# Kernel tuning notes

Measured on AMD Instinct MI355X. Metric: run time of the kernel, lower is better.

Reference implementation:

```python
import jax, jax.numpy as jnp
import numpy as np

# static config (matches init_kwargs)
T_K = 3      # Time_kernel
K = 3        # spatial_kernel_side_length
C = 64       # dim_hidden
H = 4        # num_head
D = 16       # dim_head
NL = 2       # num_layers
F = 3        # dim_feature
N, S1, S2 = 32, 32, 32
P = K // 2
L1 = T_K // 2
M = T_K * K * K
EPS = 1e-5


def _neighbor_mask():
    # spatial_neighbor_mask with an all-ones city mask: offset (k1,k2) is a valid
    # neighbor of cell (s1,s2) iff it lands inside the grid.
    m = np.zeros((S1, S2, K, K), dtype=bool)
    s1 = np.arange(S1); s2 = np.arange(S2)
    for k1 in range(K):
        v1 = (s1 + k1 - P >= 0) & (s1 + k1 - P < S1)
        for k2 in range(K):
            v2 = (s2 + k2 - P >= 0) & (s2 + k2 - P < S2)
            m[:, :, k1, k2] = v1[:, None] & v2[None, :]
    mf = m.reshape(S1, S2, K * K)
    # tiled across Time_kernel, flattened in (t, k1, k2) order like the torch code
    return np.tile(mf[:, :, None, :], (1, 1, T_K, 1)).reshape(S1, S2, M)

_MASK = jnp.asarray(_neighbor_mask())


def _forward(x, W_in, b_in, W_out, b_out, Wq, bq, Wk, bk, Wv, bv):
    # BatchNorm2d (training-mode batch stats, affine = identity init)
    mean = x.mean(axis=(0, 1, 2))
    var = ((x - mean) ** 2).mean(axis=(0, 1, 2))
    h = (x - mean) * jax.lax.rsqrt(var + EPS)
    h = h @ W_in + b_in  # [N,S1,S2,C]

    for l in range(NL):
        res = h  # res_block_thickness = 1 -> residual every layer
        q = (h @ Wq[l] + bq[l]).reshape(N, S1, S2, H, D)
        # spatial unfold (nn.Unfold, padding=K//2, stride=1)
        hp = jnp.pad(h, ((0, 0), (P, P), (P, P), (0, 0)))
        u = jnp.stack([jnp.stack([hp[:, k1:k1 + S1, k2:k2 + S2, :]
                                  for k2 in range(K)]) for k1 in range(K)])  # [K,K,N,S1,S2,C]
        # time unfold (zero-padded shifts along N)
        up = jnp.pad(u, ((0, 0), (0, 0), (L1, L1), (0, 0), (0, 0), (0, 0)))
        ut = jnp.stack([up[:, :, t:t + N] for t in range(T_K)])  # [T,K,K,N,S1,S2,C]
        # per-offset single-Linear MLPs (kernel_neurons=[C,C]), batched over T,K,K
        ks = jnp.einsum('tijnabc,tijcd->nabtijd', ut, Wk[l]) + bk[l]
        vs = jnp.einsum('tijnabc,tijcd->nabtijd', ut, Wv[l]) + bv[l]
        kM = ks.reshape(N, S1, S2, M, H, D)
        vM = vs.reshape(N, S1, S2, M, H, D)
        # unscaled dot-product attention over valid neighbors (masked == dropped)
        sc = jnp.einsum('nabmhd,nabhd->nabhm', kM, q)
        sc = jnp.where(_MASK[None, :, :, None, :], sc, -1e30)
        w = jax.nn.softmax(sc, axis=-1)
        h = jnp.einsum('nabhm,nabmhd->nabhd', w, vM).reshape(N, S1, S2, C)
        h = h + res

    return h @ W_out + b_out  # [N,S1,S2,F]


def setup_inputs() -> dict:
    key = jax.random.key(0)
    k = jax.random.split(key, 11)
    s = 0.05
    return {
        'x': jax.random.normal(k[0], (N, S1, S2, F), jnp.float32),
        'W_in': jax.random.normal(k[1], (F, C), jnp.float32) * s,
        'b_in': jax.random.normal(k[2], (C,), jnp.float32) * s,
        'W_out': jax.random.normal(k[3], (C, F), jnp.float32) * s,
        'b_out': jax.random.normal(k[4], (F,), jnp.float32) * s,
        'Wq': jax.random.normal(k[5], (NL, C, C), jnp.float32) * s,
        'bq': jax.random.normal(k[6], (NL, C), jnp.float32) * s,
        'Wk': jax.random.normal(k[7], (NL, T_K, K, K, C, C), jnp.float32) * s,
        'bk': jax.random.normal(k[8], (NL, T_K, K, K, C), jnp.float32) * s,
        'Wv': jax.random.normal(k[9], (NL, T_K, K, K, C, C), jnp.float32) * s,
        'bv': jax.random.normal(k[10], (NL, T_K, K, K, C), jnp.float32) * s,
    }


def reference(x, W_in, b_in, W_out, b_out, Wq, bq, Wk, bk, Wv, bv):
    return _forward(x, W_in, b_in, W_out, b_out, Wq, bq, Wk, bk, Wv, bv)
```

## Files before the change

### kernel.cpp

```cpp
#include <hip/hip_runtime.h>
#include <hip/hip_bf16.h>


typedef short short8_t __attribute__((ext_vector_type(8)));
typedef float floatx16 __attribute__((ext_vector_type(16)));

__device__ __forceinline__ short f2bs(float f) {
    __hip_bfloat16 h = __float2bfloat16(f);
    return *reinterpret_cast<short*>(&h);
}
__device__ __forceinline__ float bs2f(short s) {
    union { unsigned u; float f; } v;
    v.u = ((unsigned)(unsigned short)s) << 16;
    return v.f;
}
__device__ __forceinline__ int hn_idx(int rowid, int chunk) {
    return rowid * 64 + ((chunk ^ (rowid & 7)) << 3);
}
__device__ __forceinline__ float half_sum(float p) {
    float a = p, b = p;
    asm("v_permlane32_swap_b32 %0, %1" : "+v"(a), "+v"(b));
    return a + b;
}

__global__ void prep_kernel(const float* __restrict__ Wq, const float* __restrict__ Wk,
                            const float* __restrict__ Wv, short* __restrict__ dst,
                            const float* __restrict__ x, float* __restrict__ sums) {
    if (blockIdx.x < 220) {
        int t = blockIdx.x * 256 + threadIdx.x;
        if (t >= 110 * 512) return;
        int mat  = t >> 9;
        int rem  = t & 511;
        int hp   = rem >> 8;
        int kk   = (rem >> 6) & 3;
        int lane = rem & 63;
        int krow = kk * 16 + ((lane >> 5) << 3);
        int col  = hp * 32 + (lane & 31);
        const float* W;
        if (mat < 2)       W = Wq + mat * 4096;
        else if (mat < 56) W = Wk + (mat - 2) * 4096;
        else               W = Wv + (mat - 56) * 4096;
        short8_t v;
        #pragma unroll
        for (int j = 0; j < 8; ++j) v[j] = f2bs(W[(krow + j) * 64 + col]);
        *(short8_t*)&dst[(size_t)mat * 4096 + ((hp * 4 + kk) * 64 + lane) * 8] = v;
    } else {
        int bid = blockIdx.x - 220;
        int t = bid * 256 + threadIdx.x;
        const float4* x4 = (const float4*)x;
        float4 v0 = x4[t * 3 + 0], v1 = x4[t * 3 + 1], v2 = x4[t * 3 + 2];
        float vv[6];
        vv[0] = v0.x + v0.w + v1.z + v2.y;
        vv[1] = v0.y + v1.x + v1.w + v2.z;
        vv[2] = v0.z + v1.y + v2.x + v2.w;
        vv[3] = v0.x*v0.x + v0.w*v0.w + v1.z*v1.z + v2.y*v2.y;
        vv[4] = v0.y*v0.y + v1.x*v1.x + v1.w*v1.w + v2.z*v2.z;
        vv[5] = v0.z*v0.z + v1.y*v1.y + v2.x*v2.x + v2.w*v2.w;
        #pragma unroll
        for (int i = 0; i < 6; ++i) {
            #pragma unroll
            for (int off = 1; off < 64; off <<= 1) vv[i] += __shfl_xor(vv[i], off);
        }
        __shared__ float part[4][6];
        if ((threadIdx.x & 63) == 0) {
            #pragma unroll
            for (int i = 0; i < 6; ++i) part[threadIdx.x >> 6][i] = vv[i];
        }
        __syncthreads();
        if (threadIdx.x < 6)
            sums[bid * 8 + threadIdx.x] = part[0][threadIdx.x] + part[1][threadIdx.x] +
                                          part[2][threadIdx.x] + part[3][threadIdx.x];
    }
}

template <bool FIRST>
__global__ __launch_bounds__(512, 4)
void layer_fused(const float* __restrict__ x, const float* __restrict__ sums,
                 const float* __restrict__ W_in, const float* __restrict__ b_in,
                 const short* __restrict__ hbf_in, short* __restrict__ hbf_out,
                 const float* __restrict__ Wout, const float* __restrict__ bout,
                 float* __restrict__ out,
                 const short* __restrict__ wqB, const float* __restrict__ bq,
                 const short* __restrict__ wkB, const float* __restrict__ bk,
                 const short* __restrict__ wvB, const float* __restrict__ bv) {
    __shared__ short HnS[216 * 64];
    __shared__ float BiasS[3456];
    __shared__ float Waux[256];
    __shared__ float bn6[6];

    const int tid = threadIdx.x;
    const int bb0 = blockIdx.x * 2, a = blockIdx.y, nb = blockIdx.z;

    if (FIRST) {
        if (tid < 3) {
            float s = 0.f, qq = 0.f;
            #pragma unroll
            for (int p = 0; p < 32; ++p) { s += sums[p * 8 + tid]; qq += sums[p * 8 + 3 + tid]; }
            float mean = s * (1.f / 32768.f);
            float var  = qq * (1.f / 32768.f) - mean * mean;
            bn6[tid]     = mean;
            bn6[3 + tid] = rsqrtf(var + 1e-5f);
        }
        if (tid < 192)      Waux[tid] = W_in[tid];
        else if (tid < 256) Waux[tid] = b_in[tid - 192];
    } else {
        if (tid < 192)      Waux[tid] = Wout[tid];
        else if (tid < 195) Waux[tid] = bout[tid - 192];
    }
    __syncthreads();

    float mean0 = 0, mean1 = 0, mean2 = 0, rs0 = 0, rs1 = 0, rs2 = 0;
    if (FIRST) {
        mean0 = bn6[0]; mean1 = bn6[1]; mean2 = bn6[2];
        rs0 = bn6[3]; rs1 = bn6[4]; rs2 = bn6[5];
    }

    for (int id = tid; id < 3456; id += 512) {
        const int half = (id >= 1728) ? 1 : 0;
        const int j = id - half * 1728;
        const float* src = half ? &bv[j] : &bk[j];
        BiasS[((j >> 6) << 7) + (half << 6) + (j & 63)] = *src;
    }

    for (int id = tid; id < 1728; id += 512) {
        int rowid = id >> 3, cc = id & 7;
        int r = rowid % 18;
        int rw = rowid / 18;
        int spa = rw >> 2, jcol = rw & 3;
        int aa = a + spa - 1, bb = bb0 + jcol - 1;
        int n  = nb * 16 + r - 1;
        short8_t v = {0, 0, 0, 0, 0, 0, 0, 0};
        if ((unsigned)n < 32u && (unsigned)aa < 32u && (unsigned)bb < 32u) {
            int cell = (n * 32 + aa) * 32 + bb;
            if (FIRST) {
                float xn0 = (x[cell*3+0] - mean0) * rs0;
                float xn1 = (x[cell*3+1] - mean1) * rs1;
                float xn2 = (x[cell*3+2] - mean2) * rs2;
                #pragma unroll
                for (int j = 0; j < 8; ++j) {
                    int c = cc * 8 + j;
                    float h = Waux[192+c] + xn0*Waux[c] + xn1*Waux[64+c] + xn2*Waux[128+c];
                    v[j] = f2bs(h);
                }
            } else {
                v = *(const short8_t*)&hbf_in[cell * 64 + cc * 8];
            }
        }
        *(short8_t*)&HnS[hn_idx(rowid, cc)] = v;
    }
    __syncthreads();

    const int lane = tid & 63;
    const int wv8  = tid >> 6;
    const int hp   = wv8 & 1;
    const int g4   = wv8 >> 1;
    const int col  = lane & 31;
    const int e    = col & 15;
    const int ci   = col >> 4;
    const int h5   = lane >> 5;

    unsigned amask = 0;
    #pragma unroll
    for (int d = 0; d < 3; ++d) if ((unsigned)(a + d - 1) < 32u) amask |= 1u << d;
    const bool vbL = (unsigned)(bb0 - 1) < 32u;
    const bool vbR = (unsigned)(bb0 + 2) < 32u;
    const unsigned vmask = (ci == 0) ? ((vbL ? 1u : 0u) | 2u | 4u)
                                     : (1u | 2u | (vbR ? 4u : 0u));

    const int elane = e + ci * 18;

    floatx16 qv;
    {
        const float* bqp = &bq[hp * 32 + 4 * h5];
        const float4 qa = *(const float4*)&bqp[0];
        const float4 qb = *(const float4*)&bqp[8];
        const float4 qc = *(const float4*)&bqp[16];
        const float4 qd = *(const float4*)&bqp[24];
        qv = floatx16{qa.x,qa.y,qa.z,qa.w, qb.x,qb.y,qb.z,qb.w,
                      qc.x,qc.y,qc.z,qc.w, qd.x,qd.y,qd.z,qd.w};
        const int hrow = (5 + ci) * 18 + e + 1;
        const int hb = hrow * 64, xr = hrow & 7;
        const short8_t b0 = *(const short8_t*)&HnS[hb + (((0 + h5) ^ xr) << 3)];
        const short8_t b1 = *(const short8_t*)&HnS[hb + (((2 + h5) ^ xr) << 3)];
        const short8_t b2 = *(const short8_t*)&HnS[hb + (((4 + h5) ^ xr) << 3)];
        const short8_t b3 = *(const short8_t*)&HnS[hb + (((6 + h5) ^ xr) << 3)];
        const short8_t* wqp = (const short8_t*)&wqB[(hp * 256 + lane) * 8];
        qv = __builtin_amdgcn_mfma_f32_32x32x16_bf16(wqp[0],   b0, qv, 0, 0, 0);
        qv = __builtin_amdgcn_mfma_f32_32x32x16_bf16(wqp[64],  b1, qv, 0, 0, 0);
        qv = __builtin_amdgcn_mfma_f32_32x32x16_bf16(wqp[128], b2, qv, 0, 0, 0);
        qv = __builtin_amdgcn_mfma_f32_32x32x16_bf16(wqp[192], b3, qv, 0, 0, 0);
    }

    floatx16 o = {0,0,0,0, 0,0,0,0, 0,0,0,0, 0,0,0,0};
    float ssA = 0.f, ssB = 0.f;

    const int mstart = g4 * 7;
    const int mend   = (g4 == 3) ? 27 : mstart + 7;

    const short* wkBase = wkB + hp * 2048 + lane * 8;
    const short* wvBase = wvB + hp * 2048 + lane * 8;

    short8_t wkX[4], wkY[4];
    #pragma unroll
    for (int j = 0; j < 4; ++j)
        wkX[j] = *(const short8_t*)&wkBase[mstart * 4096 + j * 512];

    auto body = [&](short8_t (&wkc)[4], short8_t (&wkn)[4], const int m) {
        const int mn = (m + 1 < mend) ? (m + 1) : m;
        const int t  = (m * 57) >> 9;
        const int sp = m - 9 * t;
        const int di = (sp * 11) >> 5;
        const int dj = sp - 3 * di;

        const int hrow = (di * 4 + dj) * 18 + t + elane;
        const int hb = hrow * 64, xr = hrow & 7;
        const short8_t b0 = *(const short8_t*)&HnS[hb + (((0 + h5) ^ xr) << 3)];
        const short8_t b1 = *(const short8_t*)&HnS[hb + (((2 + h5) ^ xr) << 3)];
        const short8_t b2 = *(const short8_t*)&HnS[hb + (((4 + h5) ^ xr) << 3)];
        const short8_t b3 = *(const short8_t*)&HnS[hb + (((6 + h5) ^ xr) << 3)];

        const float* bks = &BiasS[(m << 7) + (hp << 5) + (h5 << 2)];
        const float4 ka = *(const float4*)&bks[0];
        const float4 kb = *(const float4*)&bks[8];
        const float4 kc = *(const float4*)&bks[16];
        const float4 kd = *(const float4*)&bks[24];
        const float4 va0 = *(const float4*)&bks[64];
        const float4 va1 = *(const float4*)&bks[72];
        const float4 va2 = *(const float4*)&bks[80];
        const float4 va3 = *(const float4*)&bks[88];

        const short8_t wv0 = *(const short8_t*)&wvBase[m * 4096 + 0];
        const short8_t wv1 = *(const short8_t*)&wvBase[m * 4096 + 512];
        const short8_t wv2 = *(const short8_t*)&wvBase[m * 4096 + 1024];
        const short8_t wv3 = *(const short8_t*)&wvBase[m * 4096 + 1536];

        #pragma unroll
        for (int j = 0; j < 4; ++j)
            wkn[j] = *(const short8_t*)&wkBase[mn * 4096 + j * 512];

        floatx16 kacc = floatx16{ka.x,ka.y,ka.z,ka.w, kb.x,kb.y,kb.z,kb.w,
                                 kc.x,kc.y,kc.z,kc.w, kd.x,kd.y,kd.z,kd.w};
        kacc = __builtin_amdgcn_mfma_f32_32x32x16_bf16(wkc[0], b0, kacc, 0, 0, 0);
        kacc = __builtin_amdgcn_mfma_f32_32x32x16_bf16(wkc[1], b1, kacc, 0, 0, 0);
        kacc = __builtin_amdgcn_mfma_f32_32x32x16_bf16(wkc[2], b2, kacc, 0, 0, 0);
        kacc = __builtin_amdgcn_mfma_f32_32x32x16_bf16(wkc[3], b3, kacc, 0, 0, 0);

        floatx16 vacc = floatx16{va0.x,va0.y,va0.z,va0.w, va1.x,va1.y,va1.z,va1.w,
                                 va2.x,va2.y,va2.z,va2.w, va3.x,va3.y,va3.z,va3.w};
        vacc = __builtin_amdgcn_mfma_f32_32x32x16_bf16(wv0, b0, vacc, 0, 0, 0);
        vacc = __builtin_amdgcn_mfma_f32_32x32x16_bf16(wv1, b1, vacc, 0, 0, 0);
        vacc = __builtin_amdgcn_mfma_f32_32x32x16_bf16(wv2, b2, vacc, 0, 0, 0);
        vacc = __builtin_amdgcn_mfma_f32_32x32x16_bf16(wv3, b3, vacc, 0, 0, 0);

        float pA = kacc[0] * qv[0];
        #pragma unroll
        for (int r = 1; r < 8; ++r) pA += kacc[r] * qv[r];
        float pB = kacc[8] * qv[8];
        #pragma unroll
        for (int r = 9; r < 16; ++r) pB += kacc[r] * qv[r];
        pA = half_sum(pA);
        pB = half_sum(pB);
        const float mf = (float)(((amask >> di) & (vmask >> dj)) & 1u);
        const float wA = __expf(pA) * mf;
        const float wB = __expf(pB) * mf;
        ssA += wA; ssB += wB;
        #pragma unroll
        for (int r = 0; r < 8; ++r)  o[r] += wA * vacc[r];
        #pragma unroll
        for (int r = 8; r < 16; ++r) o[r] += wB * vacc[r];
    };

    for (int m = mstart; m < mend; m += 2) {
        body(wkX, wkY, m);
        if (m + 1 < mend) body(wkY, wkX, m + 1);
    }

    __syncthreads();
    float* stbuf = (float*)HnS;
    if (g4 >= 2) {
        float* d = &stbuf[(((g4 - 2) * 2 + hp) * 64 + lane) * 20];
        *(float4*)&d[0]  = make_float4(o[0],  o[1],  o[2],  o[3]);
        *(float4*)&d[4]  = make_float4(o[4],  o[5],  o[6],  o[7]);
        *(float4*)&d[8]  = make_float4(o[8],  o[9],  o[10], o[11]);
        *(float4*)&d[12] = make_float4(o[12], o[13], o[14], o[15]);
        *(float2*)&d[16] = make_float2(ssA, ssB);
    }
    __syncthreads();
    if (g4 < 2) {
        const float* d = &stbuf[((g4 * 2 + hp) * 64 + lane) * 20];
        const float4 r0 = *(const float4*)&d[0];
        const float4 r1 = *(const float4*)&d[4];
        const float4 r2 = *(const float4*)&d[8];
        const float4 r3 = *(const float4*)&d[12];
        const float2 rs = *(const float2*)&d[16];
        o[0] += r0.x; o[1] += r0.y; o[2]  += r0.z; o[3]  += r0.w;
        o[4] += r1.x; o[5] += r1.y; o[6]  += r1.z; o[7]  += r1.w;
        o[8] += r2.x; o[9] += r2.y; o[10] += r2.z; o[11] += r2.w;
        o[12] += r3.x; o[13] += r3.y; o[14] += r3.z; o[15] += r3.w;
        ssA += rs.x; ssB += rs.y;
    }
    __syncthreads();
    if (g4 == 1) {
        float* d = &stbuf[(hp * 64 + lane) * 20];
        *(float4*)&d[0]  = make_float4(o[0],  o[1],  o[2],  o[3]);
        *(float4*)&d[4]  = make_float4(o[4],  o[5],  o[6],  o[7]);
        *(float4*)&d[8]  = make_float4(o[8],  o[9],  o[10], o[11]);
        *(float4*)&d[12] = make_float4(o[12], o[13], o[14], o[15]);
        *(float2*)&d[16] = make_float2(ssA, ssB);
    }
    __syncthreads();
    if (g4 == 0) {
        const float* d = &stbuf[(hp * 64 + lane) * 20];
        const float4 r0 = *(const float4*)&d[0];
        const float4 r1 = *(const float4*)&d[4];
        const float4 r2 = *(const float4*)&d[8];
        const float4 r3 = *(const float4*)&d[12];
        const float2 rs = *(const float2*)&d[16];
        o[0] += r0.x; o[1] += r0.y; o[2]  += r0.z; o[3]  += r0.w;
        o[4] += r1.x; o[5] += r1.y; o[6]  += r1.z; o[7]  += r1.w;
        o[8] += r2.x; o[9] += r2.y; o[10] += r2.z; o[11] += r2.w;
        o[12] += r3.x; o[13] += r3.y; o[14] += r3.z; o[15] += r3.w;
        ssA += rs.x; ssB += rs.y;
        const float invA = 1.0f / ssA;
        const float invB = 1.0f / ssB;
        #pragma unroll
        for (int r = 0; r < 8; ++r)  o[r] *= invA;
        #pragma unroll
        for (int r = 8; r < 16; ++r) o[r] *= invB;
    }

    const int n = nb * 16 + e;
    if (FIRST) {
        if (g4 == 0) {
            const int cell = (n * 32 + a) * 32 + bb0 + ci;
            const float xn0 = (x[cell*3+0] - mean0) * rs0;
            const float xn1 = (x[cell*3+1] - mean1) * rs1;
            const float xn2 = (x[cell*3+2] - mean2) * rs2;
            #pragma unroll
            for (int g = 0; g < 4; ++g) {
                short4 hb4; short* hbp = (short*)&hb4;
                #pragma unroll
                for (int i = 0; i < 4; ++i) {
                    const int c = hp * 32 + g * 8 + 4 * h5 + i;
                    const float res = Waux[192+c] + xn0*Waux[c] + xn1*Waux[64+c] + xn2*Waux[128+c];
                    hbp[i] = f2bs(o[g * 4 + i] + res);
                }
                *(short4*)&hbf_out[cell * 64 + hp * 32 + g * 8 + 4 * h5] = hb4;
            }
        }
    } else {
        __syncthreads();
        float* hf = (float*)HnS;
        if (g4 == 0) {
            const int cell = (n * 32 + a) * 32 + bb0 + ci;
            #pragma unroll
            for (int g = 0; g < 4; ++g) {
                const short4 hb4 = *(const short4*)&hbf_in[cell * 64 + hp * 32 + g * 8 + 4 * h5];
                float4 tv = make_float4(o[g*4+0] + bs2f(hb4.x), o[g*4+1] + bs2f(hb4.y),
                                        o[g*4+2] + bs2f(hb4.z), o[g*4+3] + bs2f(hb4.w));
                *(float4*)&hf[col * 68 + hp * 32 + g * 8 + 4 * h5] = tv;
            }
        }
        __syncthreads();
        if (tid < 384) {
            const int oid = tid >> 2, part = tid & 3;
            const int rowglob = oid / 3, f = oid - rowglob * 3;
            const int cstart = part << 4;
            float acc = 0.f;
            #pragma unroll
            for (int cc = 0; cc < 16; ++cc)
                acc += hf[rowglob * 68 + cstart + cc] * Waux[(cstart + cc) * 3 + f];
            acc += __shfl_xor(acc, 1);
            acc += __shfl_xor(acc, 2);
            if (part == 0) {
                const int cio = rowglob >> 4, row = rowglob & 15;
                out[(((nb * 16 + row) * 32 + a) * 32 + bb0 + cio) * 3 + f] =
                    acc + Waux[192 + f];
            }
        }
    }
}

extern "C" void kernel_launch(void* const* d_in, const int* in_sizes, int n_in,
                              void* d_out, int out_size, void* d_ws, size_t ws_size,
                              hipStream_t stream) {
    const float* x     = (const float*)d_in[0];
    const float* W_in  = (const float*)d_in[1];
    const float* b_in  = (const float*)d_in[2];
    const float* W_out = (const float*)d_in[3];
    const float* b_out = (const float*)d_in[4];
    const float* Wq    = (const float*)d_in[5];
    const float* bq    = (const float*)d_in[6];
    const float* Wk    = (const float*)d_in[7];
    const float* bk    = (const float*)d_in[8];
    const float* Wv    = (const float*)d_in[9];
    const float* bv    = (const float*)d_in[10];

    float* ws    = (float*)d_ws;
    float* sums  = ws;
    short* h1bf  = (short*)(ws + 256);
    short* wB    = h1bf + 2097152;
    float* out   = (float*)d_out;

    prep_kernel<<<252, 256, 0, stream>>>(Wq, Wk, Wv, wB, x, sums);

    const short* wq0 = wB;                const short* wq1 = wB + 4096;
    const short* wk0 = wB + 2 * 4096;     const short* wk1 = wB + (2 + 27) * 4096;
    const short* wv0 = wB + 56 * 4096;    const short* wv1 = wB + (56 + 27) * 4096;

    dim3 grid(16, 32, 2);
    layer_fused<true><<<grid, 512, 0, stream>>>(
        x, sums, W_in, b_in, nullptr, h1bf, nullptr, nullptr, nullptr,
        wq0, bq, wk0, bk, wv0, bv);
    layer_fused<false><<<grid, 512, 0, stream>>>(
        nullptr, nullptr, nullptr, nullptr, h1bf, nullptr, W_out, b_out, out,
        wq1, bq + 64, wk1, bk + 1728, wv1, bv + 1728);
}
```

Baseline: 143.4 us.

## Prefetch both K and V weights one step ahead; stage prep weights through LDS

The main loop now double-buffers the V weight fragments as well as the K fragments, loading the next offset's Wk and Wv while the current MFMAs run, so global-load latency is hidden behind compute. Launch bounds drop from 4 to 3 waves per SIMD to make room for the extra registers, which lowers occupancy. The prep kernel now uses one block per matrix, staging the matrix in shared memory with coalesced float4 loads before the strided bf16 repack, and the grid shrinks to match.

```diff
diff --git a/kernel.cpp b/kernel.cpp
--- a/kernel.cpp
+++ b/kernel.cpp
@@ -26,26 +26,33 @@
 __global__ void prep_kernel(const float* __restrict__ Wq, const float* __restrict__ Wk,
                             const float* __restrict__ Wv, short* __restrict__ dst,
                             const float* __restrict__ x, float* __restrict__ sums) {
-    if (blockIdx.x < 220) {
-        int t = blockIdx.x * 256 + threadIdx.x;
-        if (t >= 110 * 512) return;
-        int mat  = t >> 9;
-        int rem  = t & 511;
-        int hp   = rem >> 8;
-        int kk   = (rem >> 6) & 3;
-        int lane = rem & 63;
-        int krow = kk * 16 + ((lane >> 5) << 3);
-        int col  = hp * 32 + (lane & 31);
+    if (blockIdx.x < 110) {
+        __shared__ float Wf[4096];
+        const int mat = blockIdx.x;
         const float* W;
         if (mat < 2)       W = Wq + mat * 4096;
         else if (mat < 56) W = Wk + (mat - 2) * 4096;
         else               W = Wv + (mat - 56) * 4096;
-        short8_t v;
+        const float4* W4 = (const float4*)W;
         #pragma unroll
-        for (int j = 0; j < 8; ++j) v[j] = f2bs(W[(krow + j) * 64 + col]);
-        *(short8_t*)&dst[(size_t)mat * 4096 + ((hp * 4 + kk) * 64 + lane) * 8] = v;
+        for (int i = 0; i < 4; ++i) {
+            const int idx = threadIdx.x + i * 256;
+            *(float4*)&Wf[idx * 4] = W4[idx];
+        }
+        __syncthreads();
+        #pragma unroll
+        for (int u = 0; u < 2; ++u) {
+            const int t2 = u * 256 + threadIdx.x;
+            const int hp = t2 >> 8, kk = (t2 >> 6) & 3, lane = t2 & 63;
+            const int krow = kk * 16 + ((lane >> 5) << 3);
+            const int col  = hp * 32 + (lane & 31);
+            short8_t v;
+            #pragma unroll
+            for (int j = 0; j < 8; ++j) v[j] = f2bs(Wf[(krow + j) * 64 + col]);
+            *(short8_t*)&dst[(size_t)mat * 4096 + t2 * 8] = v;
+        }
     } else {
-        int bid = blockIdx.x - 220;
+        int bid = blockIdx.x - 110;
         int t = bid * 256 + threadIdx.x;
         const float4* x4 = (const float4*)x;
         float4 v0 = x4[t * 3 + 0], v1 = x4[t * 3 + 1], v2 = x4[t * 3 + 2];
@@ -74,7 +81,7 @@
 }
 
 template <bool FIRST>
-__global__ __launch_bounds__(512, 4)
+__global__ __launch_bounds__(512, 3)
 void layer_fused(const float* __restrict__ x, const float* __restrict__ sums,
                  const float* __restrict__ W_in, const float* __restrict__ b_in,
                  const short* __restrict__ hbf_in, short* __restrict__ hbf_out,
@@ -200,80 +207,89 @@
     const short* wkBase = wkB + hp * 2048 + lane * 8;
     const short* wvBase = wvB + hp * 2048 + lane * 8;
 
-    short8_t wkX[4], wkY[4];
-    #pragma unroll
-    for (int j = 0; j < 4; ++j)
-        wkX[j] = *(const short8_t*)&wkBase[mstart * 4096 + j * 512];
-
-    auto body = [&](short8_t (&wkc)[4], short8_t (&wkn)[4], const int m) {
-        const int mn = (m + 1 < mend) ? (m + 1) : m;
-        const int t  = (m * 57) >> 9;
-        const int sp = m - 9 * t;
-        const int di = (sp * 11) >> 5;
-        const int dj = sp - 3 * di;
-
-        const int hrow = (di * 4 + dj) * 18 + t + elane;
-        const int hb = hrow * 64, xr = hrow & 7;
-        const short8_t b0 = *(const short8_t*)&HnS[hb + (((0 + h5) ^ xr) << 3)];
-        const short8_t b1 = *(const short8_t*)&HnS[hb + (((2 + h5) ^ xr) << 3)];
-        const short8_t b2 = *(const short8_t*)&HnS[hb + (((4 + h5) ^ xr) << 3)];
-        const short8_t b3 = *(const short8_t*)&HnS[hb + (((6 + h5) ^ xr) << 3)];
-
-        const float* bks = &BiasS[(m << 7) + (hp << 5) + (h5 << 2)];
-        const float4 ka = *(const float4*)&bks[0];
-        const float4 kb = *(const float4*)&bks[8];
-        const float4 kc = *(const float4*)&bks[16];
-        const float4 kd = *(const float4*)&bks[24];
-        const float4 va0 = *(const float4*)&bks[64];
-        const float4 va1 = *(const float4*)&bks[72];
-        const float4 va2 = *(const float4*)&bks[80];
-        const float4 va3 = *(const float4*)&bks[88];
-
-        const short8_t wv0 = *(const short8_t*)&wvBase[m * 4096 + 0];
-        const short8_t wv1 = *(const short8_t*)&wvBase[m * 4096 + 512];
-        const short8_t wv2 = *(const short8_t*)&wvBase[m * 4096 + 1024];
-        const short8_t wv3 = *(const short8_t*)&wvBase[m * 4096 + 1536];
-
-        #pragma unroll
-        for (int j = 0; j < 4; ++j)
-            wkn[j] = *(const short8_t*)&wkBase[mn * 4096 + j * 512];
-
-        floatx16 kacc = floatx16{ka.x,ka.y,ka.z,ka.w, kb.x,kb.y,kb.z,kb.w,
-                                 kc.x,kc.y,kc.z,kc.w, kd.x,kd.y,kd.z,kd.w};
-        kacc = __builtin_amdgcn_mfma_f32_32x32x16_bf16(wkc[0], b0, kacc, 0, 0, 0);
-        kacc = __builtin_amdgcn_mfma_f32_32x32x16_bf16(wkc[1], b1, kacc, 0, 0, 0);
-        kacc = __builtin_amdgcn_mfma_f32_32x32x16_bf16(wkc[2], b2, kacc, 0, 0, 0);
-        kacc = __builtin_amdgcn_mfma_f32_32x32x16_bf16(wkc[3], b3, kacc, 0, 0, 0);
-
-        floatx16 vacc = floatx16{va0.x,va0.y,va0.z,va0.w, va1.x,va1.y,va1.z,va1.w,
-                                 va2.x,va2.y,va2.z,va2.w, va3.x,va3.y,va3.z,va3.w};
-        vacc = __builtin_amdgcn_mfma_f32_32x32x16_bf16(wv0, b0, vacc, 0, 0, 0);
-        vacc = __builtin_amdgcn_mfma_f32_32x32x16_bf16(wv1, b1, vacc, 0, 0, 0);
-        vacc = __builtin_amdgcn_mfma_f32_32x32x16_bf16(wv2, b2, vacc, 0, 0, 0);
-        vacc = __builtin_amdgcn_mfma_f32_32x32x16_bf16(wv3, b3, vacc, 0, 0, 0);
-
-        float pA = kacc[0] * qv[0];
-        #pragma unroll
-        for (int r = 1; r < 8; ++r) pA += kacc[r] * qv[r];
-        float pB = kacc[8] * qv[8];
-        #pragma unroll
-        for (int r = 9; r < 16; ++r) pB += kacc[r] * qv[r];
-        pA = half_sum(pA);
-        pB = half_sum(pB);
-        const float mf = (float)(((amask >> di) & (vmask >> dj)) & 1u);
-        const float wA = __expf(pA) * mf;
-        const float wB = __expf(pB) * mf;
-        ssA += wA; ssB += wB;
-        #pragma unroll
-        for (int r = 0; r < 8; ++r)  o[r] += wA * vacc[r];
-        #pragma unroll
-        for (int r = 8; r < 16; ++r) o[r] += wB * vacc[r];
-    };
+    short8_t wkP0, wkP1, wkP2, wkP3, wvP0, wvP1, wvP2, wvP3;
+    short8_t wkQ0, wkQ1, wkQ2, wkQ3, wvQ0, wvQ1, wvQ2, wvQ3;
+    wkP0 = *(const short8_t*)&wkBase[mstart * 4096 + 0];
+    wkP1 = *(const short8_t*)&wkBase[mstart * 4096 + 512];
+    wkP2 = *(const short8_t*)&wkBase[mstart * 4096 + 1024];
+    wkP3 = *(const short8_t*)&wkBase[mstart * 4096 + 1536];
+    wvP0 = *(const short8_t*)&wvBase[mstart * 4096 + 0];
+    wvP1 = *(const short8_t*)&wvBase[mstart * 4096 + 512];
+    wvP2 = *(const short8_t*)&wvBase[mstart * 4096 + 1024];
+    wvP3 = *(const short8_t*)&wvBase[mstart * 4096 + 1536];
+
+#define KV_BODY(WKC0,WKC1,WKC2,WKC3, WVC0,WVC1,WVC2,WVC3,                          \
+                WKN0,WKN1,WKN2,WKN3, WVN0,WVN1,WVN2,WVN3, MV)                      \
+    {                                                                              \
+        const int m_  = (MV);                                                      \
+        const int mn_ = (m_ + 1 < mend) ? m_ + 1 : m_;                             \
+        const int t_  = (m_ * 57) >> 9;                                            \
+        const int sp_ = m_ - 9 * t_;                                               \
+        const int di_ = (sp_ * 11) >> 5;                                           \
+        const int dj_ = sp_ - 3 * di_;                                             \
+        const int hrow_ = (di_ * 4 + dj_) * 18 + t_ + elane;                       \
+        const int hb_ = hrow_ * 64, xr_ = hrow_ & 7;                               \
+        const short8_t b0_ = *(const short8_t*)&HnS[hb_ + (((0 + h5) ^ xr_) << 3)];\
+        const short8_t b1_ = *(const short8_t*)&HnS[hb_ + (((2 + h5) ^ xr_) << 3)];\
+        const short8_t b2_ = *(const short8_t*)&HnS[hb_ + (((4 + h5) ^ xr_) << 3)];\
+        const short8_t b3_ = *(const short8_t*)&HnS[hb_ + (((6 + h5) ^ xr_) << 3)];\
+        const float* bks_ = &BiasS[(m_ << 7) + (hp << 5) + (h5 << 2)];             \
+        const float4 ka_ = *(const float4*)&bks_[0];                               \
+        const float4 kb_ = *(const float4*)&bks_[8];                               \
+        const float4 kc_ = *(const float4*)&bks_[16];                              \
+        const float4 kd_ = *(const float4*)&bks_[24];                              \
+        const float4 va0_ = *(const float4*)&bks_[64];                             \
+        const float4 va1_ = *(const float4*)&bks_[72];                             \
+        const float4 va2_ = *(const float4*)&bks_[80];                             \
+        const float4 va3_ = *(const float4*)&bks_[88];                             \
+        WKN0 = *(const short8_t*)&wkBase[mn_ * 4096 + 0];                          \
+        WKN1 = *(const short8_t*)&wkBase[mn_ * 4096 + 512];                        \
+        WKN2 = *(const short8_t*)&wkBase[mn_ * 4096 + 1024];                       \
+        WKN3 = *(const short8_t*)&wkBase[mn_ * 4096 + 1536];                       \
+        WVN0 = *(const short8_t*)&wvBase[mn_ * 4096 + 0];                          \
+        WVN1 = *(const short8_t*)&wvBase[mn_ * 4096 + 512];                        \
+        WVN2 = *(const short8_t*)&wvBase[mn_ * 4096 + 1024];                       \
+        WVN3 = *(const short8_t*)&wvBase[mn_ * 4096 + 1536];                       \
+        floatx16 kacc_ = floatx16{ka_.x,ka_.y,ka_.z,ka_.w, kb_.x,kb_.y,kb_.z,kb_.w,\
+                                  kc_.x,kc_.y,kc_.z,kc_.w, kd_.x,kd_.y,kd_.z,kd_.w};\
+        kacc_ = __builtin_amdgcn_mfma_f32_32x32x16_bf16(WKC0, b0_, kacc_, 0, 0, 0);\
+        kacc_ = __builtin_amdgcn_mfma_f32_32x32x16_bf16(WKC1, b1_, kacc_, 0, 0, 0);\
+        kacc_ = __builtin_amdgcn_mfma_f32_32x32x16_bf16(WKC2, b2_, kacc_, 0, 0, 0);\
+        kacc_ = __builtin_amdgcn_mfma_f32_32x32x16_bf16(WKC3, b3_, kacc_, 0, 0, 0);\
+        floatx16 vacc_ = floatx16{va0_.x,va0_.y,va0_.z,va0_.w,                     \
+                                  va1_.x,va1_.y,va1_.z,va1_.w,                     \
+                                  va2_.x,va2_.y,va2_.z,va2_.w,                     \
+                                  va3_.x,va3_.y,va3_.z,va3_.w};                    \
+        vacc_ = __builtin_amdgcn_mfma_f32_32x32x16_bf16(WVC0, b0_, vacc_, 0, 0, 0);\
+        vacc_ = __builtin_amdgcn_mfma_f32_32x32x16_bf16(WVC1, b1_, vacc_, 0, 0, 0);\
+        vacc_ = __builtin_amdgcn_mfma_f32_32x32x16_bf16(WVC2, b2_, vacc_, 0, 0, 0);\
+        vacc_ = __builtin_amdgcn_mfma_f32_32x32x16_bf16(WVC3, b3_, vacc_, 0, 0, 0);\
+        float pA_ = kacc_[0] * qv[0];                                              \
+        _Pragma("unroll")                                                          \
+        for (int r = 1; r < 8; ++r) pA_ += kacc_[r] * qv[r];                       \
+        float pB_ = kacc_[8] * qv[8];                                              \
+        _Pragma("unroll")                                                          \
+        for (int r = 9; r < 16; ++r) pB_ += kacc_[r] * qv[r];                      \
+        pA_ = half_sum(pA_);                                                       \
+        pB_ = half_sum(pB_);                                                       \
+        const float mf_ = (float)(((amask >> di_) & (vmask >> dj_)) & 1u);         \
+        const float wA_ = __expf(pA_) * mf_;                                       \
+        const float wB_ = __expf(pB_) * mf_;                                       \
+        ssA += wA_; ssB += wB_;                                                    \
+        _Pragma("unroll")                                                          \
+        for (int r = 0; r < 8; ++r)  o[r] += wA_ * vacc_[r];                       \
+        _Pragma("unroll")                                                          \
+        for (int r = 8; r < 16; ++r) o[r] += wB_ * vacc_[r];                       \
+    }
 
     for (int m = mstart; m < mend; m += 2) {
-        body(wkX, wkY, m);
-        if (m + 1 < mend) body(wkY, wkX, m + 1);
-    }
+        KV_BODY(wkP0,wkP1,wkP2,wkP3, wvP0,wvP1,wvP2,wvP3,
+                wkQ0,wkQ1,wkQ2,wkQ3, wvQ0,wvQ1,wvQ2,wvQ3, m)
+        if (m + 1 < mend)
+        KV_BODY(wkQ0,wkQ1,wkQ2,wkQ3, wvQ0,wvQ1,wvQ2,wvQ3,
+                wkP0,wkP1,wkP2,wkP3, wvP0,wvP1,wvP2,wvP3, m + 1)
+    }
+#undef KV_BODY
 
     __syncthreads();
     float* stbuf = (float*)HnS;
@@ -402,7 +418,7 @@
     short* wB    = h1bf + 2097152;
     float* out   = (float*)d_out;
 
-    prep_kernel<<<252, 256, 0, stream>>>(Wq, Wk, Wv, wB, x, sums);
+    prep_kernel<<<142, 256, 0, stream>>>(Wq, Wk, Wv, wB, x, sums);
 
     const short* wq0 = wB;                const short* wq1 = wB + 4096;
     const short* wk0 = wB + 2 * 4096;     const short* wk1 = wB + (2 + 27) * 4096;
```

Result: slower. 153.3 us (+6.9%).

## Give each wave full offset loop over more cells instead of splitting offsets

Applied to the files above, without the earlier changes.

The layer kernel drops the split of the 27 neighbour offsets across four wave groups and the LDS tree reduction that merged their partial outputs. Each block now handles four columns with 256 threads, and each wave loops over all 27 offsets for its own cells, using a larger halo tile in LDS. This removes the cross-wave reduction syncs and the extra LDS traffic, and halves the grid, at the cost of a longer serial loop per wave, fewer blocks, and dropping the explicit wk register prefetch. The prep kernel now stages each weight matrix through LDS with coalesced float4 loads before repacking it to bf16.

```diff
diff --git a/kernel.cpp b/kernel.cpp
--- a/kernel.cpp
+++ b/kernel.cpp
@@ -26,26 +26,33 @@
 __global__ void prep_kernel(const float* __restrict__ Wq, const float* __restrict__ Wk,
                             const float* __restrict__ Wv, short* __restrict__ dst,
                             const float* __restrict__ x, float* __restrict__ sums) {
-    if (blockIdx.x < 220) {
-        int t = blockIdx.x * 256 + threadIdx.x;
-        if (t >= 110 * 512) return;
-        int mat  = t >> 9;
-        int rem  = t & 511;
-        int hp   = rem >> 8;
-        int kk   = (rem >> 6) & 3;
-        int lane = rem & 63;
-        int krow = kk * 16 + ((lane >> 5) << 3);
-        int col  = hp * 32 + (lane & 31);
+    if (blockIdx.x < 110) {
+        __shared__ float Wf[4096];
+        const int mat = blockIdx.x;
         const float* W;
         if (mat < 2)       W = Wq + mat * 4096;
         else if (mat < 56) W = Wk + (mat - 2) * 4096;
         else               W = Wv + (mat - 56) * 4096;
-        short8_t v;
-        #pragma unroll
-        for (int j = 0; j < 8; ++j) v[j] = f2bs(W[(krow + j) * 64 + col]);
-        *(short8_t*)&dst[(size_t)mat * 4096 + ((hp * 4 + kk) * 64 + lane) * 8] = v;
+        const float4* W4 = (const float4*)W;
+        #pragma unroll
+        for (int i = 0; i < 4; ++i) {
+            const int idx = threadIdx.x + i * 256;
+            *(float4*)&Wf[idx * 4] = W4[idx];
+        }
+        __syncthreads();
+        #pragma unroll
+        for (int u = 0; u < 2; ++u) {
+            const int t2 = u * 256 + threadIdx.x;
+            const int hp = t2 >> 8, kk = (t2 >> 6) & 3, lane = t2 & 63;
+            const int krow = kk * 16 + ((lane >> 5) << 3);
+            const int col  = hp * 32 + (lane & 31);
+            short8_t v;
+            #pragma unroll
+            for (int j = 0; j < 8; ++j) v[j] = f2bs(Wf[(krow + j) * 64 + col]);
+            *(short8_t*)&dst[(size_t)mat * 4096 + t2 * 8] = v;
+        }
     } else {
-        int bid = blockIdx.x - 220;
+        int bid = blockIdx.x - 110;
         int t = bid * 256 + threadIdx.x;
         const float4* x4 = (const float4*)x;
         float4 v0 = x4[t * 3 + 0], v1 = x4[t * 3 + 1], v2 = x4[t * 3 + 2];
@@ -74,7 +81,7 @@
 }
 
 template <bool FIRST>
-__global__ __launch_bounds__(512, 4)
+__global__ __launch_bounds__(256, 2)
 void layer_fused(const float* __restrict__ x, const float* __restrict__ sums,
                  const float* __restrict__ W_in, const float* __restrict__ b_in,
                  const short* __restrict__ hbf_in, short* __restrict__ hbf_out,
@@ -83,13 +90,13 @@
                  const short* __restrict__ wqB, const float* __restrict__ bq,
                  const short* __restrict__ wkB, const float* __restrict__ bk,
                  const short* __restrict__ wvB, const float* __restrict__ bv) {
-    __shared__ short HnS[216 * 64];
+    __shared__ short HnS[324 * 64];
     __shared__ float BiasS[3456];
     __shared__ float Waux[256];
     __shared__ float bn6[6];
 
     const int tid = threadIdx.x;
-    const int bb0 = blockIdx.x * 2, a = blockIdx.y, nb = blockIdx.z;
+    const int bb0 = blockIdx.x * 4, a = blockIdx.y, nb = blockIdx.z;
 
     if (FIRST) {
         if (tid < 3) {
@@ -101,8 +108,8 @@
             bn6[tid]     = mean;
             bn6[3 + tid] = rsqrtf(var + 1e-5f);
         }
-        if (tid < 192)      Waux[tid] = W_in[tid];
-        else if (tid < 256) Waux[tid] = b_in[tid - 192];
+        if (tid < 192) Waux[tid] = W_in[tid];
+        else           Waux[tid] = b_in[tid - 192];
     } else {
         if (tid < 192)      Waux[tid] = Wout[tid];
         else if (tid < 195) Waux[tid] = bout[tid - 192];
@@ -115,18 +122,18 @@
         rs0 = bn6[3]; rs1 = bn6[4]; rs2 = bn6[5];
     }
 
-    for (int id = tid; id < 3456; id += 512) {
+    for (int id = tid; id < 3456; id += 256) {
         const int half = (id >= 1728) ? 1 : 0;
         const int j = id - half * 1728;
         const float* src = half ? &bv[j] : &bk[j];
         BiasS[((j >> 6) << 7) + (half << 6) + (j & 63)] = *src;
     }
 
-    for (int id = tid; id < 1728; id += 512) {
+    for (int id = tid; id < 2592; id += 256) {
         int rowid = id >> 3, cc = id & 7;
         int r = rowid % 18;
         int rw = rowid / 18;
-        int spa = rw >> 2, jcol = rw & 3;
+        int spa = rw / 6, jcol = rw - spa * 6;
         int aa = a + spa - 1, bb = bb0 + jcol - 1;
         int n  = nb * 16 + r - 1;
         short8_t v = {0, 0, 0, 0, 0, 0, 0, 0};
@@ -151,23 +158,24 @@
     __syncthreads();
 
     const int lane = tid & 63;
-    const int wv8  = tid >> 6;
-    const int hp   = wv8 & 1;
-    const int g4   = wv8 >> 1;
+    const int wv4  = tid >> 6;
+    const int hp   = wv4 & 1;
+    const int cg   = wv4 >> 1;
     const int col  = lane & 31;
     const int e    = col & 15;
     const int ci   = col >> 4;
     const int h5   = lane >> 5;
+    const int cell4 = cg * 2 + ci;
+    const int bcell = bb0 + cell4;
 
     unsigned amask = 0;
     #pragma unroll
     for (int d = 0; d < 3; ++d) if ((unsigned)(a + d - 1) < 32u) amask |= 1u << d;
-    const bool vbL = (unsigned)(bb0 - 1) < 32u;
-    const bool vbR = (unsigned)(bb0 + 2) < 32u;
-    const unsigned vmask = (ci == 0) ? ((vbL ? 1u : 0u) | 2u | 4u)
-                                     : (1u | 2u | (vbR ? 4u : 0u));
-
-    const int elane = e + ci * 18;
+    unsigned vmask = 0;
+    #pragma unroll
+    for (int j = 0; j < 3; ++j) if ((unsigned)(bcell + j - 1) < 32u) vmask |= 1u << j;
+
+    const int elane = cell4 * 18 + e;
 
     floatx16 qv;
     {
@@ -178,7 +186,7 @@
         const float4 qd = *(const float4*)&bqp[24];
         qv = floatx16{qa.x,qa.y,qa.z,qa.w, qb.x,qb.y,qb.z,qb.w,
                       qc.x,qc.y,qc.z,qc.w, qd.x,qd.y,qd.z,qd.w};
-        const int hrow = (5 + ci) * 18 + e + 1;
+        const int hrow = (7 + cell4) * 18 + e + 1;
         const int hb = hrow * 64, xr = hrow & 7;
         const short8_t b0 = *(const short8_t*)&HnS[hb + (((0 + h5) ^ xr) << 3)];
         const short8_t b1 = *(const short8_t*)&HnS[hb + (((2 + h5) ^ xr) << 3)];
@@ -194,25 +202,17 @@
     floatx16 o = {0,0,0,0, 0,0,0,0, 0,0,0,0, 0,0,0,0};
     float ssA = 0.f, ssB = 0.f;
 
-    const int mstart = g4 * 7;
-    const int mend   = (g4 == 3) ? 27 : mstart + 7;
-
     const short* wkBase = wkB + hp * 2048 + lane * 8;
     const short* wvBase = wvB + hp * 2048 + lane * 8;
 
-    short8_t wkX[4], wkY[4];
-    #pragma unroll
-    for (int j = 0; j < 4; ++j)
-        wkX[j] = *(const short8_t*)&wkBase[mstart * 4096 + j * 512];
-
-    auto body = [&](short8_t (&wkc)[4], short8_t (&wkn)[4], const int m) {
-        const int mn = (m + 1 < mend) ? (m + 1) : m;
+    #pragma unroll 3
+    for (int m = 0; m < 27; ++m) {
         const int t  = (m * 57) >> 9;
         const int sp = m - 9 * t;
         const int di = (sp * 11) >> 5;
         const int dj = sp - 3 * di;
 
-        const int hrow = (di * 4 + dj) * 18 + t + elane;
+        const int hrow = di * 108 + dj * 18 + t + elane;
         const int hb = hrow * 64, xr = hrow & 7;
         const short8_t b0 = *(const short8_t*)&HnS[hb + (((0 + h5) ^ xr) << 3)];
         const short8_t b1 = *(const short8_t*)&HnS[hb + (((2 + h5) ^ xr) << 3)];
@@ -229,21 +229,21 @@
         const float4 va2 = *(const float4*)&bks[80];
         const float4 va3 = *(const float4*)&bks[88];
 
+        const short8_t wk0 = *(const short8_t*)&wkBase[m * 4096 + 0];
+        const short8_t wk1 = *(const short8_t*)&wkBase[m * 4096 + 512];
+        const short8_t wk2 = *(const short8_t*)&wkBase[m * 4096 + 1024];
+        const short8_t wk3 = *(const short8_t*)&wkBase[m * 4096 + 1536];
         const short8_t wv0 = *(const short8_t*)&wvBase[m * 4096 + 0];
         const short8_t wv1 = *(const short8_t*)&wvBase[m * 4096 + 512];
         const short8_t wv2 = *(const short8_t*)&wvBase[m * 4096 + 1024];
         const short8_t wv3 = *(const short8_t*)&wvBase[m * 4096 + 1536];
 
-        #pragma unroll
-        for (int j = 0; j < 4; ++j)
-            wkn[j] = *(const short8_t*)&wkBase[mn * 4096 + j * 512];
-
         floatx16 kacc = floatx16{ka.x,ka.y,ka.z,ka.w, kb.x,kb.y,kb.z,kb.w,
                                  kc.x,kc.y,kc.z,kc.w, kd.x,kd.y,kd.z,kd.w};
-        kacc = __builtin_amdgcn_mfma_f32_32x32x16_bf16(wkc[0], b0, kacc, 0, 0, 0);
-        kacc = __builtin_amdgcn_mfma_f32_32x32x16_bf16(wkc[1], b1, kacc, 0, 0, 0);
-        kacc = __builtin_amdgcn_mfma_f32_32x32x16_bf16(wkc[2], b2, kacc, 0, 0, 0);
-        kacc = __builtin_amdgcn_mfma_f32_32x32x16_bf16(wkc[3], b3, kacc, 0, 0, 0);
+        kacc = __builtin_amdgcn_mfma_f32_32x32x16_bf16(wk0, b0, kacc, 0, 0, 0);
+        kacc = __builtin_amdgcn_mfma_f32_32x32x16_bf16(wk1, b1, kacc, 0, 0, 0);
+        kacc = __builtin_amdgcn_mfma_f32_32x32x16_bf16(wk2, b2, kacc, 0, 0, 0);
+        kacc = __builtin_amdgcn_mfma_f32_32x32x16_bf16(wk3, b3, kacc, 0, 0, 0);
 
         floatx16 vacc = floatx16{va0.x,va0.y,va0.z,va0.w, va1.x,va1.y,va1.z,va1.w,
                                  va2.x,va2.y,va2.z,va2.w, va3.x,va3.y,va3.z,va3.w};
@@ -268,59 +268,9 @@
         for (int r = 0; r < 8; ++r)  o[r] += wA * vacc[r];
         #pragma unroll
         for (int r = 8; r < 16; ++r) o[r] += wB * vacc[r];
-    };
-
-    for (int m = mstart; m < mend; m += 2) {
-        body(wkX, wkY, m);
-        if (m + 1 < mend) body(wkY, wkX, m + 1);
-    }
-
-    __syncthreads();
-    float* stbuf = (float*)HnS;
-    if (g4 >= 2) {
-        float* d = &stbuf[(((g4 - 2) * 2 + hp) * 64 + lane) * 20];
-        *(float4*)&d[0]  = make_float4(o[0],  o[1],  o[2],  o[3]);
-        *(float4*)&d[4]  = make_float4(o[4],  o[5],  o[6],  o[7]);
-        *(float4*)&d[8]  = make_float4(o[8],  o[9],  o[10], o[11]);
-        *(float4*)&d[12] = make_float4(o[12], o[13], o[14], o[15]);
-        *(float2*)&d[16] = make_float2(ssA, ssB);
-    }
-    __syncthreads();
-    if (g4 < 2) {
-        const float* d = &stbuf[((g4 * 2 + hp) * 64 + lane) * 20];
-        const float4 r0 = *(const float4*)&d[0];
-        const float4 r1 = *(const float4*)&d[4];
-        const float4 r2 = *(const float4*)&d[8];
-        const float4 r3 = *(const float4*)&d[12];
-        const float2 rs = *(const float2*)&d[16];
-        o[0] += r0.x; o[1] += r0.y; o[2]  += r0.z; o[3]  += r0.w;
-        o[4] += r1.x; o[5] += r1.y; o[6]  += r1.z; o[7]  += r1.w;
-        o[8] += r2.x; o[9] += r2.y; o[10] += r2.z; o[11] += r2.w;
-        o[12] += r3.x; o[13] += r3.y; o[14] += r3.z; o[15] += r3.w;
-        ssA += rs.x; ssB += rs.y;
-    }
-    __syncthreads();
-    if (g4 == 1) {
-        float* d = &stbuf[(hp * 64 + lane) * 20];
-        *(float4*)&d[0]  = make_float4(o[0],  o[1],  o[2],  o[3]);
-        *(float4*)&d[4]  = make_float4(o[4],  o[5],  o[6],  o[7]);
-        *(float4*)&d[8]  = make_float4(o[8],  o[9],  o[10], o[11]);
-        *(float4*)&d[12] = make_float4(o[12], o[13], o[14], o[15]);
-        *(float2*)&d[16] = make_float2(ssA, ssB);
-    }
-    __syncthreads();
-    if (g4 == 0) {
-        const float* d = &stbuf[(hp * 64 + lane) * 20];
-        const float4 r0 = *(const float4*)&d[0];
-        const float4 r1 = *(const float4*)&d[4];
-        const float4 r2 = *(const float4*)&d[8];
-        const float4 r3 = *(const float4*)&d[12];
-        const float2 rs = *(const float2*)&d[16];
-        o[0] += r0.x; o[1] += r0.y; o[2]  += r0.z; o[3]  += r0.w;
-        o[4] += r1.x; o[5] += r1.y; o[6]  += r1.z; o[7]  += r1.w;
-        o[8] += r2.x; o[9] += r2.y; o[10] += r2.z; o[11] += r2.w;
-        o[12] += r3.x; o[13] += r3.y; o[14] += r3.z; o[15] += r3.w;
-        ssA += rs.x; ssB += rs.y;
+    }
+
+    {
         const float invA = 1.0f / ssA;
         const float invB = 1.0f / ssB;
         #pragma unroll
@@ -330,53 +280,41 @@
     }
 
     const int n = nb * 16 + e;
+    const int cell = (n * 32 + a) * 32 + bcell;
     if (FIRST) {
-        if (g4 == 0) {
-            const int cell = (n * 32 + a) * 32 + bb0 + ci;
-            const float xn0 = (x[cell*3+0] - mean0) * rs0;
-            const float xn1 = (x[cell*3+1] - mean1) * rs1;
-            const float xn2 = (x[cell*3+2] - mean2) * rs2;
-            #pragma unroll
-            for (int g = 0; g < 4; ++g) {
-                short4 hb4; short* hbp = (short*)&hb4;
-                #pragma unroll
-                for (int i = 0; i < 4; ++i) {
-                    const int c = hp * 32 + g * 8 + 4 * h5 + i;
-                    const float res = Waux[192+c] + xn0*Waux[c] + xn1*Waux[64+c] + xn2*Waux[128+c];
-                    hbp[i] = f2bs(o[g * 4 + i] + res);
-                }
-                *(short4*)&hbf_out[cell * 64 + hp * 32 + g * 8 + 4 * h5] = hb4;
+        const float xn0 = (x[cell*3+0] - mean0) * rs0;
+        const float xn1 = (x[cell*3+1] - mean1) * rs1;
+        const float xn2 = (x[cell*3+2] - mean2) * rs2;
+        #pragma unroll
+        for (int g = 0; g < 4; ++g) {
+            short4 hb4; short* hbp = (short*)&hb4;
+            #pragma unroll
+            for (int i = 0; i < 4; ++i) {
+                const int c = hp * 32 + g * 8 + 4 * h5 + i;
+                const float res = Waux[192+c] + xn0*Waux[c] + xn1*Waux[64+c] + xn2*Waux[128+c];
+                hbp[i] = f2bs(o[g * 4 + i] + res);
             }
+            *(short4*)&hbf_out[cell * 64 + hp * 32 + g * 8 + 4 * h5] = hb4;
         }
     } else {
         __syncthreads();
         float* hf = (float*)HnS;
-        if (g4 == 0) {
-            const int cell = (n * 32 + a) * 32 + bb0 + ci;
-            #pragma unroll
-            for (int g = 0; g < 4; ++g) {
-                const short4 hb4 = *(const short4*)&hbf_in[cell * 64 + hp * 32 + g * 8 + 4 * h5];
-                float4 tv = make_float4(o[g*4+0] + bs2f(hb4.x), o[g*4+1] + bs2f(hb4.y),
-                                        o[g*4+2] + bs2f(hb4.z), o[g*4+3] + bs2f(hb4.w));
-                *(float4*)&hf[col * 68 + hp * 32 + g * 8 + 4 * h5] = tv;
-            }
+        const int bcol = cell4 * 16 + e;
+        #pragma unroll
+        for (int g = 0; g < 4; ++g) {
+            const short4 hb4 = *(const short4*)&hbf_in[cell * 64 + hp * 32 + g * 8 + 4 * h5];
+            float4 tv = make_float4(o[g*4+0] + bs2f(hb4.x), o[g*4+1] + bs2f(hb4.y),
+                                    o[g*4+2] + bs2f(hb4.z), o[g*4+3] + bs2f(hb4.w));
+            *(float4*)&hf[bcol * 68 + hp * 32 + g * 8 + 4 * h5] = tv;
         }
         __syncthreads();
-        if (tid < 384) {
-            const int oid = tid >> 2, part = tid & 3;
-            const int rowglob = oid / 3, f = oid - rowglob * 3;
-            const int cstart = part << 4;
-            float acc = 0.f;
-            #pragma unroll
-            for (int cc = 0; cc < 16; ++cc)
-                acc += hf[rowglob * 68 + cstart + cc] * Waux[(cstart + cc) * 3 + f];
-            acc += __shfl_xor(acc, 1);
-            acc += __shfl_xor(acc, 2);
-            if (part == 0) {
-                const int cio = rowglob >> 4, row = rowglob & 15;
-                out[(((nb * 16 + row) * 32 + a) * 32 + bb0 + cio) * 3 + f] =
-                    acc + Waux[192 + f];
-            }
+        if (tid < 192) {
+            const int rowglob = tid / 3, f = tid - rowglob * 3;
+            float acc = Waux[192 + f];
+            #pragma unroll 8
+            for (int cc = 0; cc < 64; ++cc) acc += hf[rowglob * 68 + cc] * Waux[cc * 3 + f];
+            const int cellb = bb0 + (rowglob >> 4), row = rowglob & 15;
+            out[(((nb * 16 + row) * 32 + a) * 32 + cellb) * 3 + f] = acc;
         }
     }
 }
@@ -402,17 +340,17 @@
     short* wB    = h1bf + 2097152;
     float* out   = (float*)d_out;
 
-    prep_kernel<<<252, 256, 0, stream>>>(Wq, Wk, Wv, wB, x, sums);
+    prep_kernel<<<142, 256, 0, stream>>>(Wq, Wk, Wv, wB, x, sums);
 
     const short* wq0 = wB;                const short* wq1 = wB + 4096;
     const short* wk0 = wB + 2 * 4096;     const short* wk1 = wB + (2 + 27) * 4096;
     const short* wv0 = wB + 56 * 4096;    const short* wv1 = wB + (56 + 27) * 4096;
 
-    dim3 grid(16, 32, 2);
-    layer_fused<true><<<grid, 512, 0, stream>>>(
+    dim3 grid(8, 32, 2);
+    layer_fused<true><<<grid, 256, 0, stream>>>(
         x, sums, W_in, b_in, nullptr, h1bf, nullptr, nullptr, nullptr,
         wq0, bq, wk0, bk, wv0, bv);
-    layer_fused<false><<<grid, 512, 0, stream>>>(
+    layer_fused<false><<<grid, 256, 0, stream>>>(
         nullptr, nullptr, nullptr, nullptr, h1bf, nullptr, W_out, b_out, out,
         wq1, bq + 64, wk1, bk + 1728, wv1, bv + 1728);
 }
```

New measurement: 133.7 us. -6.7%, faster.
